# Performance work log

Hardware: AMD Instinct MI355X
Metric: run time of the kernel (lower is better)

Reference implementation:

```python
import jax, jax.numpy as jnp
import numpy as np
from jax import lax

N_ITER = 5
SMOOTHNESS_WEIGHT = 1.0
SMOOTHNESS_THETA = 1.0
FILTER_SIZE = 11  # crfseg-style default odd Gaussian filter size


def _gaussian_kernel_1d():
    c = (FILTER_SIZE - 1) / 2.0
    d = jnp.arange(FILTER_SIZE, dtype=jnp.float32) - c
    k = jnp.exp(-(d ** 2) / (2.0 * SMOOTHNESS_THETA ** 2))
    return k / jnp.sum(k)


def _blur(q):
    # q: (B, C, H, W); separable per-channel Gaussian smoothing, 'same' padding
    B, C, H, W = q.shape
    k = _gaussian_kernel_1d()
    r = q.reshape(B * C, 1, H, W)
    dn = ('NCHW', 'OIHW', 'NCHW')
    r = lax.conv_general_dilated(r, k.reshape(1, 1, FILTER_SIZE, 1), (1, 1), 'SAME', dimension_numbers=dn)
    r = lax.conv_general_dilated(r, k.reshape(1, 1, 1, FILTER_SIZE), (1, 1), 'SAME', dimension_numbers=dn)
    return r.reshape(B, C, H, W)


def setup_inputs() -> dict:
    key = jax.random.key(0)
    k1, k2 = jax.random.split(key)
    x = jax.random.normal(k1, (16, 3, 512, 512), dtype=jnp.float32)
    conv_w = jax.random.normal(k2, (2, 3, 3, 3), dtype=jnp.float32) * 0.1
    conv_b = jnp.zeros((2,), dtype=jnp.float32)
    return {"x": x, "conv_w": conv_w, "conv_b": conv_b}


def reference(x, conv_w, conv_b):
    # backbone: simple 3x3 conv producing per-class logits (B, C, H, W)
    dn = ('NCHW', 'OIHW', 'NCHW')
    logits = lax.conv_general_dilated(x, conv_w, (1, 1), 'SAME', dimension_numbers=dn)
    logits = logits + conv_b[None, :, None, None]

    # mean-field CRF: compatibility mu(k,k') = -(k==k') => message = -blur(q)
    unary = logits
    cur = logits
    for _ in range(N_ITER):
        q = jax.nn.softmax(cur, axis=1)
        cur = unary + SMOOTHNESS_WEIGHT * _blur(q)
    return cur
```

## Files before the change

### kernel.cpp

```cpp
#include <hip/hip_runtime.h>

constexpr int BB = 16;
constexpr int HH = 512;
constexpr int WW = 512;
constexpr int HW = HH * WW;
constexpr int NP1 = BB * HW;

using half_t = _Float16;
using half2v = __attribute__((ext_vector_type(2))) _Float16;
using half8v = __attribute__((ext_vector_type(8))) _Float16;

__device__ __forceinline__ half2v hfma2(half2v a, half2v b, half2v c) {
#if __has_builtin(__builtin_elementwise_fma)
    return __builtin_elementwise_fma(a, b, c);
#else
    return a * b + c;
#endif
}

__device__ constexpr float GK[11] = {
    1.4867195147342977e-06f,
    1.3383022576488537e-04f,
    4.4318484119380075e-03f,
    5.3990966513188063e-02f,
    2.4197072451914337e-01f,
    3.9894228040143270e-01f,
    2.4197072451914337e-01f,
    5.3990966513188063e-02f,
    4.4318484119380075e-03f,
    1.3383022576488537e-04f,
    1.4867195147342977e-06f,
};
__device__ constexpr float PFX[6] = {
    0.0f,
    1.4867195147342977e-06f,
    1.3531694527962e-04f,
    4.5671653572176e-03f,
    5.8558131870406e-02f,
    3.0052885638955e-01f,
};

__device__ __forceinline__ float edgeS(int i) {
    float s = 1.f;
    if (i < 5)   s -= PFX[5 - i];
    if (i > 506) s -= PFX[i - 506];
    return s;
}

__device__ __forceinline__ float sig1(float d) {
    d = fminf(fmaxf(d, -30.f), 30.f);
    float e = __expf(d);
    return e * __builtin_amdgcn_rcpf(1.f + e);
}

__device__ __forceinline__ half2v hblur_pk(const half_t* vr, int tid) {
    const unsigned int* vd = (const unsigned int*)vr;
    unsigned int D[7];
#pragma unroll
    for (int k = 0; k < 7; ++k) D[k] = vd[tid + k];
    half2v m01 = half2v{(half_t)0.f, (half_t)0.f};
#pragma unroll
    for (int t = 0; t < 11; ++t) {
        unsigned int P;
        if (t & 1) P = D[(t + 1) >> 1];
        else       P = (D[t >> 1] >> 16) | (D[(t >> 1) + 1] << 16);
        half2v Ph = __builtin_bit_cast(half2v, P);
        half_t kh = (half_t)GK[t];
        half2v kv = half2v{kh, kh};
        m01 = hfma2(kv, Ph, m01);
    }
    return m01;
}

__global__ __launch_bounds__(256) void conv3x3_duq(
    const float* __restrict__ x, const float* __restrict__ w,
    const float* __restrict__ bias, half_t* __restrict__ u0p,
    half_t* __restrict__ dup, half_t* __restrict__ q0p)
{
    int bid = blockIdx.x;
    int sb  = (bid & 7) * 128 + (bid >> 3);
    int t   = sb * 256 + threadIdx.x;
    int b   = t >> 14;
    int rem = t & 16383;
    int y0  = (rem >> 6) << 1;
    int xs  = (rem & 63) << 3;

    float W[54];
#pragma unroll
    for (int i = 0; i < 13; ++i)
        *(float4*)&W[4 * i] = *(const float4*)(w + 4 * i);
    W[52] = w[52];
    W[53] = w[53];
    float b0 = bias[0], b1 = bias[1];

    float acc0[2][8], acc1[2][8];
#pragma unroll
    for (int r = 0; r < 2; ++r)
#pragma unroll
        for (int j = 0; j < 8; ++j) { acc0[r][j] = b0; acc1[r][j] = b1; }

    const float* xb = x + (size_t)b * 3 * HW;
#pragma unroll
    for (int ci = 0; ci < 3; ++ci) {
        const float* xc = xb + ci * HW;
#pragma unroll
        for (int iy = 0; iy < 4; ++iy) {
            int yy = y0 - 1 + iy;
            if (yy < 0 || yy >= HH) continue;
            const float* r = xc + yy * WW;
            float4 cA = *(const float4*)(r + xs);
            float4 cB = *(const float4*)(r + xs + 4);
            float l  = (xs > 0)      ? r[xs - 1] : 0.f;
            float rr = (xs < WW - 8) ? r[xs + 8] : 0.f;
            float v[10] = {l, cA.x, cA.y, cA.z, cA.w,
                           cB.x, cB.y, cB.z, cB.w, rr};
#pragma unroll
            for (int orow = 0; orow < 2; ++orow) {
                int kh = iy - orow;
                if (kh < 0 || kh > 2) continue;
                float w00 = W[ci * 9 + kh * 3 + 0];
                float w01 = W[ci * 9 + kh * 3 + 1];
                float w02 = W[ci * 9 + kh * 3 + 2];
                float w10 = W[27 + ci * 9 + kh * 3 + 0];
                float w11 = W[27 + ci * 9 + kh * 3 + 1];
                float w12 = W[27 + ci * 9 + kh * 3 + 2];
#pragma unroll
                for (int j = 0; j < 8; ++j) {
                    acc0[orow][j] = fmaf(w00, v[j],
                                    fmaf(w01, v[j + 1],
                                    fmaf(w02, v[j + 2], acc0[orow][j])));
                    acc1[orow][j] = fmaf(w10, v[j],
                                    fmaf(w11, v[j + 1],
                                    fmaf(w12, v[j + 2], acc1[orow][j])));
                }
            }
        }
    }
#pragma unroll
    for (int orow = 0; orow < 2; ++orow) {
        size_t o = (size_t)b * HW + (size_t)(y0 + orow) * WW + xs;
        half8v h0, h1, hq;
#pragma unroll
        for (int j = 0; j < 8; ++j) {
            float du = acc1[orow][j] - acc0[orow][j];
            h0[j] = (half_t)acc0[orow][j];
            h1[j] = (half_t)du;
            hq[j] = (half_t)sig1(du);
        }
        *(half8v*)(u0p + o) = h0;
        *(half8v*)(dup + o) = h1;
        *(half8v*)(q0p + o) = hq;
    }
}

__global__ __launch_bounds__(256) void q_iter(
    const half_t* __restrict__ qp, const half_t* __restrict__ dup,
    half_t* __restrict__ qnxt)
{
    __shared__ half_t v[4][528];

    int bid  = blockIdx.x;
    int tile = (bid & 7) * 256 + (bid >> 3);
    int b    = tile >> 7;
    int y0   = (tile & 127) << 2;
    int tid  = threadIdx.x;
    int x0   = tid << 1;

    if (tid < 6) {
#pragma unroll
        for (int r = 0; r < 4; ++r) {
            v[r][tid] = (half_t)0.f;
            v[r][518 + tid] = (half_t)0.f;
        }
    }

    size_t pb = (size_t)b * HW + x0;

    half2v acc[4];
#pragma unroll
    for (int r = 0; r < 4; ++r) acc[r] = half2v{(half_t)0.f, (half_t)0.f};

#pragma unroll
    for (int i = 0; i < 14; ++i) {
        int yy = y0 + i - 5;
        if (yy < 0 || yy >= HH) continue;
        half2v qv = *(const half2v*)(qp + pb + (size_t)yy * WW);
#pragma unroll
        for (int r = 0; r < 4; ++r) {
            int dt = i - r;
            if (dt < 0 || dt > 10) continue;
            half_t kh = (half_t)GK[dt];
            half2v kv = half2v{kh, kh};
            acc[r] = hfma2(kv, qv, acc[r]);
        }
    }
#pragma unroll
    for (int r = 0; r < 4; ++r)
        *(half2v*)(&v[r][6 + x0]) = acc[r];
    __syncthreads();

    float SxA = edgeS(x0), SxB = edgeS(x0 + 1);

#pragma unroll
    for (int r = 0; r < 4; ++r) {
        int yy = y0 + r;
        float Sy = edgeS(yy);

        half2v m01h = hblur_pk(&v[r][0], tid);
        float m0 = (float)m01h[0], m1 = (float)m01h[1];

        size_t po = pb + (size_t)yy * WW;
        half2v duv = *(const half2v*)(dup + po);
        float d0 = (float)duv[0] + fmaf(2.f, m0, -(SxA * Sy));
        float d1 = (float)duv[1] + fmaf(2.f, m1, -(SxB * Sy));

        half2v hq;
        hq[0] = (half_t)sig1(d0);
        hq[1] = (half_t)sig1(d1);
        *(half2v*)(qnxt + po) = hq;
    }
}

__global__ __launch_bounds__(256) void q_final(
    const half_t* __restrict__ qp, const half_t* __restrict__ dup,
    const half_t* __restrict__ u0p, float* __restrict__ outp)
{
    __shared__ half_t v[4][528];

    int bid  = blockIdx.x;
    int tile = (bid & 7) * 256 + (bid >> 3);
    int b    = tile >> 7;
    int y0   = (tile & 127) << 2;
    int tid  = threadIdx.x;
    int x0   = tid << 1;

    if (tid < 6) {
#pragma unroll
        for (int r = 0; r < 4; ++r) {
            v[r][tid] = (half_t)0.f;
            v[r][518 + tid] = (half_t)0.f;
        }
    }

    size_t pb = (size_t)b * HW + x0;

    half2v acc[4];
#pragma unroll
    for (int r = 0; r < 4; ++r) acc[r] = half2v{(half_t)0.f, (half_t)0.f};

#pragma unroll
    for (int i = 0; i < 14; ++i) {
        int yy = y0 + i - 5;
        if (yy < 0 || yy >= HH) continue;
        half2v qv = *(const half2v*)(qp + pb + (size_t)yy * WW);
#pragma unroll
        for (int r = 0; r < 4; ++r) {
            int dt = i - r;
            if (dt < 0 || dt > 10) continue;
            half_t kh = (half_t)GK[dt];
            half2v kv = half2v{kh, kh};
            acc[r] = hfma2(kv, qv, acc[r]);
        }
    }
#pragma unroll
    for (int r = 0; r < 4; ++r)
        *(half2v*)(&v[r][6 + x0]) = acc[r];
    __syncthreads();

    float SxA = edgeS(x0), SxB = edgeS(x0 + 1);

#pragma unroll
    for (int r = 0; r < 4; ++r) {
        int yy = y0 + r;
        float Sy = edgeS(yy);

        half2v m01h = hblur_pk(&v[r][0], tid);
        float m0 = (float)m01h[0], m1 = (float)m01h[1];

        size_t po = pb + (size_t)yy * WW;
        half2v duv = *(const half2v*)(dup + po);
        half2v u0v = *(const half2v*)(u0p + po);
        float dua = (float)duv[0], dub = (float)duv[1];
        float ua  = (float)u0v[0], ub  = (float)u0v[1];

        float S0 = SxA * Sy, S1 = SxB * Sy;
        size_t oo = (size_t)b * 2 * HW + (size_t)yy * WW + x0;
        *(float2*)(outp + oo)      = make_float2(ua + (S0 - m0),
                                                 ub + (S1 - m1));
        *(float2*)(outp + oo + HW) = make_float2((ua + dua) + m0,
                                                 (ub + dub) + m1);
    }
}

extern "C" void kernel_launch(void* const* d_in, const int* in_sizes, int n_in,
                              void* d_out, int out_size, void* d_ws, size_t ws_size,
                              hipStream_t stream) {
    const float* x    = (const float*)d_in[0];
    const float* w    = (const float*)d_in[1];
    const float* bias = (const float*)d_in[2];

    float*  out = (float*)d_out;
    half_t* u0p = (half_t*)d_ws;
    half_t* dup = u0p + NP1;
    half_t* qA  = dup + NP1;
    half_t* qB  = qA + NP1;

    conv3x3_duq<<<1024, 256, 0, stream>>>(x, w, bias, u0p, dup, qA);
    q_iter<<<2048, 256, 0, stream>>>(qA, dup, qB);
    q_iter<<<2048, 256, 0, stream>>>(qB, dup, qA);
    q_iter<<<2048, 256, 0, stream>>>(qA, dup, qB);
    q_iter<<<2048, 256, 0, stream>>>(qB, dup, qA);
    q_final<<<2048, 256, 0, stream>>>(qA, dup, u0p, out);
}
```

Before: 67.59 us.

## Fuse two CRF mean-field iterations per kernel with halo recompute

Replaces pairs of q_iter launches with a q_pair kernel that computes two consecutive mean-field iterations on an 8-row tile. It recomputes an 18-row intermediate halo in shared memory instead of writing the intermediate q to global memory and reading it back. This removes two kernel launches and one full global round-trip of q per pair. In exchange it does redundant halo compute (18 rows for 8 outputs), uses more shared memory (about 38KB) and more registers, and launches half as many blocks.

```diff
diff --git a/kernel.cpp b/kernel.cpp
--- a/kernel.cpp
+++ b/kernel.cpp
@@ -153,9 +153,114 @@
     }
 }
 
-__global__ __launch_bounds__(256) void q_iter(
+__global__ __launch_bounds__(256) void q_pair(
+    const half_t* __restrict__ qin, const half_t* __restrict__ dup,
+    half_t* __restrict__ qout)
+{
+    __shared__ half_t va[18][528];
+    __shared__ half_t qq[18][528];
+
+    int bid  = blockIdx.x;
+    int tile = (bid & 7) * 128 + (bid >> 3);
+    int b    = tile >> 6;
+    int y0   = (tile & 63) << 3;
+    int tid  = threadIdx.x;
+    int x0   = tid << 1;
+
+    if (tid < 6) {
+#pragma unroll
+        for (int r = 0; r < 18; ++r) {
+            va[r][tid] = (half_t)0.f;
+            va[r][518 + tid] = (half_t)0.f;
+        }
+    }
+
+    size_t pb = (size_t)b * HW + x0;
+    float SxA = edgeS(x0), SxB = edgeS(x0 + 1);
+
+    half2v acc[18];
+#pragma unroll
+    for (int r = 0; r < 18; ++r) acc[r] = half2v{(half_t)0.f, (half_t)0.f};
+#pragma unroll
+    for (int i = 0; i < 28; ++i) {
+        int yy = y0 + i - 10;
+        if (yy < 0 || yy >= HH) continue;
+        half2v qv = *(const half2v*)(qin + pb + (size_t)yy * WW);
+#pragma unroll
+        for (int r1 = 0; r1 < 18; ++r1) {
+            int dt = i - r1;
+            if (dt < 0 || dt > 10) continue;
+            half_t kh = (half_t)GK[dt];
+            half2v kv = half2v{kh, kh};
+            acc[r1] = hfma2(kv, qv, acc[r1]);
+        }
+    }
+#pragma unroll
+    for (int r1 = 0; r1 < 18; ++r1)
+        *(half2v*)(&va[r1][6 + x0]) = acc[r1];
+    __syncthreads();
+
+    half2v duo[8];
+#pragma unroll
+    for (int r1 = 0; r1 < 18; ++r1) {
+        int yy = y0 + r1 - 5;
+        if (yy >= 0 && yy < HH) {
+            half2v m01h = hblur_pk(&va[r1][0], tid);
+            float m0 = (float)m01h[0], m1 = (float)m01h[1];
+            half2v duv = *(const half2v*)(dup + pb + (size_t)yy * WW);
+            if (r1 >= 5 && r1 < 13) duo[r1 - 5] = duv;
+            float Sy = edgeS(yy);
+            float d0 = (float)duv[0] + fmaf(2.f, m0, -(SxA * Sy));
+            float d1 = (float)duv[1] + fmaf(2.f, m1, -(SxB * Sy));
+            half2v hq;
+            hq[0] = (half_t)sig1(d0);
+            hq[1] = (half_t)sig1(d1);
+            *(half2v*)(&qq[r1][6 + x0]) = hq;
+        } else {
+            *(half2v*)(&qq[r1][6 + x0]) = half2v{(half_t)0.f, (half_t)0.f};
+        }
+    }
+    __syncthreads();
+
+    half2v acc8[8];
+#pragma unroll
+    for (int r = 0; r < 8; ++r) acc8[r] = half2v{(half_t)0.f, (half_t)0.f};
+#pragma unroll
+    for (int r1 = 0; r1 < 18; ++r1) {
+        half2v qv = *(const half2v*)(&qq[r1][6 + x0]);
+#pragma unroll
+        for (int r = 0; r < 8; ++r) {
+            int dt = r1 - r;
+            if (dt < 0 || dt > 10) continue;
+            half_t kh = (half_t)GK[dt];
+            half2v kv = half2v{kh, kh};
+            acc8[r] = hfma2(kv, qv, acc8[r]);
+        }
+    }
+    __syncthreads();
+#pragma unroll
+    for (int r = 0; r < 8; ++r)
+        *(half2v*)(&va[r][6 + x0]) = acc8[r];
+    __syncthreads();
+
+#pragma unroll
+    for (int r = 0; r < 8; ++r) {
+        int yy = y0 + r;
+        float Sy = edgeS(yy);
+        half2v m01h = hblur_pk(&va[r][0], tid);
+        float m0 = (float)m01h[0], m1 = (float)m01h[1];
+        float d0 = (float)duo[r][0] + fmaf(2.f, m0, -(SxA * Sy));
+        float d1 = (float)duo[r][1] + fmaf(2.f, m1, -(SxB * Sy));
+        half2v hq;
+        hq[0] = (half_t)sig1(d0);
+        hq[1] = (half_t)sig1(d1);
+        *(half2v*)(qout + pb + (size_t)yy * WW) = hq;
+    }
+}
+
+__global__ __launch_bounds__(256) void q_final(
     const half_t* __restrict__ qp, const half_t* __restrict__ dup,
-    half_t* __restrict__ qnxt)
+    const half_t* __restrict__ u0p, float* __restrict__ outp)
 {
     __shared__ half_t v[4][528];
 
@@ -211,74 +316,6 @@
 
         size_t po = pb + (size_t)yy * WW;
         half2v duv = *(const half2v*)(dup + po);
-        float d0 = (float)duv[0] + fmaf(2.f, m0, -(SxA * Sy));
-        float d1 = (float)duv[1] + fmaf(2.f, m1, -(SxB * Sy));
-
-        half2v hq;
-        hq[0] = (half_t)sig1(d0);
-        hq[1] = (half_t)sig1(d1);
-        *(half2v*)(qnxt + po) = hq;
-    }
-}
-
-__global__ __launch_bounds__(256) void q_final(
-    const half_t* __restrict__ qp, const half_t* __restrict__ dup,
-    const half_t* __restrict__ u0p, float* __restrict__ outp)
-{
-    __shared__ half_t v[4][528];
-
-    int bid  = blockIdx.x;
-    int tile = (bid & 7) * 256 + (bid >> 3);
-    int b    = tile >> 7;
-    int y0   = (tile & 127) << 2;
-    int tid  = threadIdx.x;
-    int x0   = tid << 1;
-
-    if (tid < 6) {
-#pragma unroll
-        for (int r = 0; r < 4; ++r) {
-            v[r][tid] = (half_t)0.f;
-            v[r][518 + tid] = (half_t)0.f;
-        }
-    }
-
-    size_t pb = (size_t)b * HW + x0;
-
-    half2v acc[4];
-#pragma unroll
-    for (int r = 0; r < 4; ++r) acc[r] = half2v{(half_t)0.f, (half_t)0.f};
-
-#pragma unroll
-    for (int i = 0; i < 14; ++i) {
-        int yy = y0 + i - 5;
-        if (yy < 0 || yy >= HH) continue;
-        half2v qv = *(const half2v*)(qp + pb + (size_t)yy * WW);
-#pragma unroll
-        for (int r = 0; r < 4; ++r) {
-            int dt = i - r;
-            if (dt < 0 || dt > 10) continue;
-            half_t kh = (half_t)GK[dt];
-            half2v kv = half2v{kh, kh};
-            acc[r] = hfma2(kv, qv, acc[r]);
-        }
-    }
-#pragma unroll
-    for (int r = 0; r < 4; ++r)
-        *(half2v*)(&v[r][6 + x0]) = acc[r];
-    __syncthreads();
-
-    float SxA = edgeS(x0), SxB = edgeS(x0 + 1);
-
-#pragma unroll
-    for (int r = 0; r < 4; ++r) {
-        int yy = y0 + r;
-        float Sy = edgeS(yy);
-
-        half2v m01h = hblur_pk(&v[r][0], tid);
-        float m0 = (float)m01h[0], m1 = (float)m01h[1];
-
-        size_t po = pb + (size_t)yy * WW;
-        half2v duv = *(const half2v*)(dup + po);
         half2v u0v = *(const half2v*)(u0p + po);
         float dua = (float)duv[0], dub = (float)duv[1];
         float ua  = (float)u0v[0], ub  = (float)u0v[1];
@@ -306,9 +343,7 @@
     half_t* qB  = qA + NP1;
 
     conv3x3_duq<<<1024, 256, 0, stream>>>(x, w, bias, u0p, dup, qA);
-    q_iter<<<2048, 256, 0, stream>>>(qA, dup, qB);
-    q_iter<<<2048, 256, 0, stream>>>(qB, dup, qA);
-    q_iter<<<2048, 256, 0, stream>>>(qA, dup, qB);
-    q_iter<<<2048, 256, 0, stream>>>(qB, dup, qA);
+    q_pair<<<1024, 256, 0, stream>>>(qA, dup, qB);
+    q_pair<<<1024, 256, 0, stream>>>(qB, dup, qA);
     q_final<<<2048, 256, 0, stream>>>(qA, dup, u0p, out);
 }
```

Result: slower. 74.63 us (+10.4%).
